# Kernel tuning notes

Measured on AMD Instinct MI355X. Metric: run time of the kernel, lower is better.

Reference implementation:

```python
import jax, jax.numpy as jnp
import numpy as np

W_OUT = 0.1     # weight for voxels outside the ROI
EXPAND = 1.2    # ROI expansion coefficient


def _compute_roi(mask):
    """Vectorized equivalent of MaskedLoss._compute_roi_ for 5D [B,1,D,H,W] masks.
    Returns roi of same shape: 1.0 inside the (expanded, clipped) bounding box of
    the foreground, W_OUT elsewhere (and everywhere if a batch item has no fg)."""
    m = mask[:, 0] > 0                      # [B, D, H, W] bool
    spatial = m.shape[1:]
    has_fg = jnp.any(m, axis=(1, 2, 3))     # [B]
    inside = []
    for ax, sh in enumerate(spatial):
        other = tuple(i + 1 for i in range(3) if i != ax)
        any_ax = jnp.any(m, axis=other)                     # [B, sh]
        mn = jnp.argmax(any_ax, axis=1).astype(jnp.float32)                      # first fg index
        mx = (sh - 1 - jnp.argmax(any_ax[:, ::-1], axis=1)).astype(jnp.float32)  # last fg index
        c = (mx + mn) * 0.5
        e = (mx - mn + 1.0) * 0.5 * EXPAND
        # int(max(0, c-e)) and int(min(sh-1, c+e)) with python int() truncation on >=0 values
        lo = jnp.maximum(0.0, jnp.floor(c - e))             # [B]
        hi = jnp.minimum(float(sh - 1), jnp.floor(c + e))   # [B], slice end is EXCLUSIVE
        coords = jnp.arange(sh, dtype=jnp.float32)
        inside.append((coords[None, :] >= lo[:, None]) & (coords[None, :] < hi[:, None]))
    box = (inside[0][:, :, None, None]
           & inside[1][:, None, :, None]
           & inside[2][:, None, None, :])                   # [B, D, H, W]
    box = box & has_fg[:, None, None, None]                 # no fg -> all W_OUT
    return jnp.where(box, 1.0, W_OUT)[:, None]              # [B, 1, D, H, W]


def setup_inputs() -> dict:
    key = jax.random.key(0)
    k1, k2, k3 = jax.random.split(key, 3)
    shape = (4, 1, 160, 160, 160)
    y_pred = jax.random.normal(k1, shape, dtype=jnp.float32)
    y_true = jax.random.normal(k2, shape, dtype=jnp.float32)
    mask = jax.random.randint(k3, shape, 0, 2, dtype=jnp.int32)
    return {"y_pred": y_pred, "y_true": y_true, "mask": mask}


def reference(y_pred, y_true, mask):
    roi = _compute_roi(mask)
    # func = MSE: mean((roi*pred - roi*true)^2)
    diff = roi * y_pred - roi * y_true
    return jnp.mean(diff * diff)
```

## Files before the change

kernel.cpp:

```cpp
#include <hip/hip_runtime.h>


namespace {
constexpr int BATCH = 4;
constexpr int DSZ = 160, HSZ = 160, WSZ = 160;
constexpr int SPATIAL = DSZ * HSZ * WSZ;
constexpr int QPB = SPATIAL / 4;
constexpr int NT = 256;
constexpr int PB = 500;
constexpr int STRIDE_Q = PB * NT;
constexpr int ITERS = QPB / STRIDE_Q;
constexpr int NPART = BATCH * PB;
constexpr int SENT_MIN = 1 << 30;
}

__device__ __forceinline__ int wred_min(int v) {
#pragma unroll
  for (int o = 32; o; o >>= 1) v = min(v, __shfl_xor(v, o));
  return v;
}
__device__ __forceinline__ int wred_max(int v) {
#pragma unroll
  for (int o = 32; o; o >>= 1) v = max(v, __shfl_xor(v, o));
  return v;
}

__global__ __launch_bounds__(NT) void ml_pass1(const int* __restrict__ mask,
                                               int* __restrict__ blockres) {
  const int b = blockIdx.y;
  const int4* m4 = reinterpret_cast<const int4*>(mask + (size_t)b * SPATIAL);

  const unsigned q0 = blockIdx.x * NT + threadIdx.x;
  const unsigned d0 = q0 / 6400u;
  const unsigned rem = q0 - d0 * 6400u;
  const unsigned h = rem / 40u;
  const int wb = (int)(rem - h * 40u) * 4;

  unsigned itermask = 0;
  int elemmask = 0;
#pragma unroll
  for (int i = 0; i < ITERS; ++i) {
    int4 v = m4[q0 + (size_t)i * STRIDE_Q];
    int e = (int)(v.x > 0) | ((int)(v.y > 0) << 1) |
            ((int)(v.z > 0) << 2) | ((int)(v.w > 0) << 3);
    elemmask |= e;
    itermask |= (e ? (1u << i) : 0u);
  }

  int dmin = SENT_MIN, dmax = -1, hmin = SENT_MIN, hmax = -1, wmin = SENT_MIN, wmax = -1;
  if (itermask) {
    int ifirst = __ffs(itermask) - 1;
    int ilast = 31 - __clz(itermask);
    dmin = (int)d0 + 20 * ifirst;
    dmax = (int)d0 + 20 * ilast;
    hmin = hmax = (int)h;
    wmin = wb + (__ffs(elemmask) - 1);
    wmax = wb + (31 - __clz(elemmask));
  }

  dmin = wred_min(dmin); dmax = wred_max(dmax);
  hmin = wred_min(hmin); hmax = wred_max(hmax);
  wmin = wred_min(wmin); wmax = wred_max(wmax);

  __shared__ int sred[4][6];
  const int wave = threadIdx.x >> 6, lane = threadIdx.x & 63;
  if (lane == 0) {
    sred[wave][0] = dmin; sred[wave][1] = dmax;
    sred[wave][2] = hmin; sred[wave][3] = hmax;
    sred[wave][4] = wmin; sred[wave][5] = wmax;
  }
  __syncthreads();
  if (threadIdx.x == 0) {
    int o[6];
    o[0] = min(min(sred[0][0], sred[1][0]), min(sred[2][0], sred[3][0]));
    o[1] = max(max(sred[0][1], sred[1][1]), max(sred[2][1], sred[3][1]));
    o[2] = min(min(sred[0][2], sred[1][2]), min(sred[2][2], sred[3][2]));
    o[3] = max(max(sred[0][3], sred[1][3]), max(sred[2][3], sred[3][3]));
    o[4] = min(min(sred[0][4], sred[1][4]), min(sred[2][4], sred[3][4]));
    o[5] = max(max(sred[0][5], sred[1][5]), max(sred[2][5], sred[3][5]));
    int* dst = blockres + ((size_t)b * PB + blockIdx.x) * 6;
#pragma unroll
    for (int k = 0; k < 6; ++k) dst[k] = o[k];
  }
}

__device__ __forceinline__ void axis_box(int mni, int mxi, int sh, int* lo_i, int* hi_i) {
  float mn = (float)mni, mx = (float)mxi;
  float c = (mx + mn) * 0.5f;
  float e = (mx - mn + 1.0f) * 0.5f * 1.2f;
  float lo = fmaxf(0.0f, floorf(c - e));
  float hi = fminf((float)(sh - 1), floorf(c + e));
  *lo_i = (int)lo;
  *hi_i = (int)hi;
}

__global__ __launch_bounds__(NT) void ml_pass2(const int* __restrict__ blockres,
                                               int* __restrict__ boxp) {
  const int b = blockIdx.x;
  int dmin = SENT_MIN, dmax = -1, hmin = SENT_MIN, hmax = -1, wmin = SENT_MIN, wmax = -1;
  for (int i = threadIdx.x; i < PB; i += NT) {
    const int* r = blockres + ((size_t)b * PB + i) * 6;
    dmin = min(dmin, r[0]); dmax = max(dmax, r[1]);
    hmin = min(hmin, r[2]); hmax = max(hmax, r[3]);
    wmin = min(wmin, r[4]); wmax = max(wmax, r[5]);
  }

  dmin = wred_min(dmin); dmax = wred_max(dmax);
  hmin = wred_min(hmin); hmax = wred_max(hmax);
  wmin = wred_min(wmin); wmax = wred_max(wmax);

  __shared__ int sred[4][6];
  const int wave = threadIdx.x >> 6, lane = threadIdx.x & 63;
  if (lane == 0) {
    sred[wave][0] = dmin; sred[wave][1] = dmax;
    sred[wave][2] = hmin; sred[wave][3] = hmax;
    sred[wave][4] = wmin; sred[wave][5] = wmax;
  }
  __syncthreads();
  if (threadIdx.x == 0) {
    int Dm = min(min(sred[0][0], sred[1][0]), min(sred[2][0], sred[3][0]));
    int DM = max(max(sred[0][1], sred[1][1]), max(sred[2][1], sred[3][1]));
    int Hm = min(min(sred[0][2], sred[1][2]), min(sred[2][2], sred[3][2]));
    int HM = max(max(sred[0][3], sred[1][3]), max(sred[2][3], sred[3][3]));
    int Wm = min(min(sred[0][4], sred[1][4]), min(sred[2][4], sred[3][4]));
    int WM = max(max(sred[0][5], sred[1][5]), max(sred[2][5], sred[3][5]));
    int out[6];
    if (DM < 0) {
      out[0] = 0; out[1] = 0; out[2] = 0; out[3] = 0; out[4] = 0; out[5] = 0;
    } else {
      axis_box(Dm, DM, DSZ, &out[0], &out[1]);
      axis_box(Hm, HM, HSZ, &out[2], &out[3]);
      axis_box(Wm, WM, WSZ, &out[4], &out[5]);
    }
    int* dst = boxp + b * 8;
#pragma unroll
    for (int k = 0; k < 6; ++k) dst[k] = out[k];
  }
}

__global__ __launch_bounds__(NT) void ml_pass3(const float* __restrict__ pred,
                                               const float* __restrict__ tru,
                                               const int* __restrict__ boxp,
                                               float* __restrict__ partials) {
  const int b = blockIdx.y;
  const int lod = boxp[b * 8 + 0], hid = boxp[b * 8 + 1];
  const int loh = boxp[b * 8 + 2], hih = boxp[b * 8 + 3];
  const int low = boxp[b * 8 + 4], hiw = boxp[b * 8 + 5];

  const float4* p4 = reinterpret_cast<const float4*>(pred + (size_t)b * SPATIAL);
  const float4* t4 = reinterpret_cast<const float4*>(tru + (size_t)b * SPATIAL);

  const unsigned q0 = blockIdx.x * NT + threadIdx.x;
  const unsigned d0 = q0 / 6400u;
  const unsigned rem = q0 - d0 * 6400u;
  const unsigned h = rem / 40u;
  const int wb = (int)(rem - h * 40u) * 4;

  const bool inh = ((int)h >= loh) & ((int)h < hih);
  const float wx = (inh & (wb + 0 >= low) & (wb + 0 < hiw)) ? 1.0f : 0.1f;
  const float wy = (inh & (wb + 1 >= low) & (wb + 1 < hiw)) ? 1.0f : 0.1f;
  const float wz = (inh & (wb + 2 >= low) & (wb + 2 < hiw)) ? 1.0f : 0.1f;
  const float ww = (inh & (wb + 3 >= low) & (wb + 3 < hiw)) ? 1.0f : 0.1f;

  float s0 = 0.0f, s1 = 0.0f, s2 = 0.0f, s3 = 0.0f;
#pragma unroll
  for (int i = 0; i < ITERS; ++i) {
    float4 pv = p4[q0 + (size_t)i * STRIDE_Q];
    float4 tv = t4[q0 + (size_t)i * STRIDE_Q];
    int d = (int)d0 + 20 * i;
    bool ind = (d >= lod) & (d < hid);
    float rx = ind ? wx : 0.1f;
    float ry = ind ? wy : 0.1f;
    float rz = ind ? wz : 0.1f;
    float rw = ind ? ww : 0.1f;
    float a;
    a = rx * pv.x - rx * tv.x; s0 = fmaf(a, a, s0);
    a = ry * pv.y - ry * tv.y; s1 = fmaf(a, a, s1);
    a = rz * pv.z - rz * tv.z; s2 = fmaf(a, a, s2);
    a = rw * pv.w - rw * tv.w; s3 = fmaf(a, a, s3);
  }
  float s = (s0 + s1) + (s2 + s3);

#pragma unroll
  for (int o = 32; o; o >>= 1) s += __shfl_xor(s, o);
  __shared__ float ls[4];
  const int wave = threadIdx.x >> 6, lane = threadIdx.x & 63;
  if (lane == 0) ls[wave] = s;
  __syncthreads();
  if (threadIdx.x == 0)
    partials[(size_t)b * PB + blockIdx.x] = ls[0] + ls[1] + ls[2] + ls[3];
}

__global__ __launch_bounds__(NT) void ml_final(const float* __restrict__ partials,
                                               float* __restrict__ out) {
  double s = 0.0;
  for (int i = threadIdx.x; i < NPART; i += NT) s += (double)partials[i];
#pragma unroll
  for (int o = 32; o; o >>= 1) s += __shfl_xor(s, o);
  __shared__ double ls[4];
  const int wave = threadIdx.x >> 6, lane = threadIdx.x & 63;
  if (lane == 0) ls[wave] = s;
  __syncthreads();
  if (threadIdx.x == 0)
    out[0] = (float)((ls[0] + ls[1] + ls[2] + ls[3]) / (double)((size_t)BATCH * SPATIAL));
}

extern "C" void kernel_launch(void* const* d_in, const int* in_sizes, int n_in,
                              void* d_out, int out_size, void* d_ws, size_t ws_size,
                              hipStream_t stream) {
  const float* y_pred = (const float*)d_in[0];
  const float* y_true = (const float*)d_in[1];
  const int*   mask   = (const int*)d_in[2];
  float* out = (float*)d_out;

  char* ws = (char*)d_ws;
  int*   blockres = (int*)(ws);
  int*   boxp     = (int*)(ws + 49152);
  float* partials = (float*)(ws + 53248);

  ml_pass1<<<dim3(PB, BATCH), NT, 0, stream>>>(mask, blockres);
  ml_pass2<<<dim3(BATCH), NT, 0, stream>>>(blockres, boxp);
  ml_pass3<<<dim3(PB, BATCH), NT, 0, stream>>>(y_pred, y_true, boxp, partials);
  ml_final<<<1, NT, 0, stream>>>(partials, out);
}
```

Measured before the change: 194.1 us.

## Fuse bbox reduction via atomics and final sum via last-block pattern

```diff
diff --git a/kernel.cpp b/kernel.cpp
--- a/kernel.cpp
+++ b/kernel.cpp
@@ -7,11 +7,28 @@
 constexpr int SPATIAL = DSZ * HSZ * WSZ;
 constexpr int QPB = SPATIAL / 4;
 constexpr int NT = 256;
-constexpr int PB = 500;
-constexpr int STRIDE_Q = PB * NT;
+constexpr int PB = 1000;
+constexpr int STRIDE_Q = PB * NT * 2;
 constexpr int ITERS = QPB / STRIDE_Q;
+constexpr int DSTEP = 80;
 constexpr int NPART = BATCH * PB;
+constexpr int TOTAL_BLOCKS = BATCH * PB;
 constexpr int SENT_MIN = 1 << 30;
+
+constexpr int WS_NEG = 0;
+constexpr int WS_MAX = 64;
+constexpr int WS_CNT = 128;
+constexpr int WS_PART = 256;
+}
+
+typedef int   vint4   __attribute__((ext_vector_type(4)));
+typedef float vfloat4 __attribute__((ext_vector_type(4)));
+
+__device__ __forceinline__ vint4 ntload_i(const vint4* p) {
+  return __builtin_nontemporal_load(p);
+}
+__device__ __forceinline__ vfloat4 ntload_f(const vfloat4* p) {
+  return __builtin_nontemporal_load(p);
 }
 
 __device__ __forceinline__ int wred_min(int v) {
@@ -25,14 +42,25 @@
   return v;
 }
 
-__global__ __launch_bounds__(NT) void ml_pass1(const int* __restrict__ mask,
-                                               int* __restrict__ blockres) {
+__global__ void ml_init(int* __restrict__ ws_i) {
+  if (threadIdx.x == 0) {
+#pragma unroll
+    for (int k = 0; k < 12; ++k) ws_i[k] = -1;
+#pragma unroll
+    for (int k = 0; k < 12; ++k) ws_i[16 + k] = -1;
+    ws_i[32] = 0;
+  }
+}
+
+__global__ __launch_bounds__(NT) void ml_bbox(const int* __restrict__ mask,
+                                              int* __restrict__ bneg,
+                                              int* __restrict__ bmax) {
   const int b = blockIdx.y;
-  const int4* m4 = reinterpret_cast<const int4*>(mask + (size_t)b * SPATIAL);
-
-  const unsigned q0 = blockIdx.x * NT + threadIdx.x;
-  const unsigned d0 = q0 / 6400u;
-  const unsigned rem = q0 - d0 * 6400u;
+  const vint4* m4 = reinterpret_cast<const vint4*>(mask + (size_t)b * SPATIAL);
+
+  const unsigned qb = (blockIdx.x * NT + threadIdx.x) * 2u;
+  const unsigned d0 = qb / 6400u;
+  const unsigned rem = qb - d0 * 6400u;
   const unsigned h = rem / 40u;
   const int wb = (int)(rem - h * 40u) * 4;
 
@@ -40,9 +68,12 @@
   int elemmask = 0;
 #pragma unroll
   for (int i = 0; i < ITERS; ++i) {
-    int4 v = m4[q0 + (size_t)i * STRIDE_Q];
-    int e = (int)(v.x > 0) | ((int)(v.y > 0) << 1) |
-            ((int)(v.z > 0) << 2) | ((int)(v.w > 0) << 3);
+    vint4 v0 = ntload_i(&m4[qb + (size_t)i * STRIDE_Q]);
+    vint4 v1 = ntload_i(&m4[qb + (size_t)i * STRIDE_Q + 1]);
+    int e = (int)(v0[0] > 0) | ((int)(v0[1] > 0) << 1) |
+            ((int)(v0[2] > 0) << 2) | ((int)(v0[3] > 0) << 3) |
+            ((int)(v1[0] > 0) << 4) | ((int)(v1[1] > 0) << 5) |
+            ((int)(v1[2] > 0) << 6) | ((int)(v1[3] > 0) << 7);
     elemmask |= e;
     itermask |= (e ? (1u << i) : 0u);
   }
@@ -51,8 +82,8 @@
   if (itermask) {
     int ifirst = __ffs(itermask) - 1;
     int ilast = 31 - __clz(itermask);
-    dmin = (int)d0 + 20 * ifirst;
-    dmax = (int)d0 + 20 * ilast;
+    dmin = (int)d0 + DSTEP * ifirst;
+    dmax = (int)d0 + DSTEP * ilast;
     hmin = hmax = (int)h;
     wmin = wb + (__ffs(elemmask) - 1);
     wmax = wb + (31 - __clz(elemmask));
@@ -71,16 +102,20 @@
   }
   __syncthreads();
   if (threadIdx.x == 0) {
-    int o[6];
-    o[0] = min(min(sred[0][0], sred[1][0]), min(sred[2][0], sred[3][0]));
-    o[1] = max(max(sred[0][1], sred[1][1]), max(sred[2][1], sred[3][1]));
-    o[2] = min(min(sred[0][2], sred[1][2]), min(sred[2][2], sred[3][2]));
-    o[3] = max(max(sred[0][3], sred[1][3]), max(sred[2][3], sred[3][3]));
-    o[4] = min(min(sred[0][4], sred[1][4]), min(sred[2][4], sred[3][4]));
-    o[5] = max(max(sred[0][5], sred[1][5]), max(sred[2][5], sred[3][5]));
-    int* dst = blockres + ((size_t)b * PB + blockIdx.x) * 6;
-#pragma unroll
-    for (int k = 0; k < 6; ++k) dst[k] = o[k];
+    int Dm = min(min(sred[0][0], sred[1][0]), min(sred[2][0], sred[3][0]));
+    int DM = max(max(sred[0][1], sred[1][1]), max(sred[2][1], sred[3][1]));
+    int Hm = min(min(sred[0][2], sred[1][2]), min(sred[2][2], sred[3][2]));
+    int HM = max(max(sred[0][3], sred[1][3]), max(sred[2][3], sred[3][3]));
+    int Wm = min(min(sred[0][4], sred[1][4]), min(sred[2][4], sred[3][4]));
+    int WM = max(max(sred[0][5], sred[1][5]), max(sred[2][5], sred[3][5]));
+    if (DM >= 0) {
+      atomicMax(&bneg[b * 3 + 0], (DSZ - 1) - Dm);
+      atomicMax(&bneg[b * 3 + 1], (HSZ - 1) - Hm);
+      atomicMax(&bneg[b * 3 + 2], (WSZ - 1) - Wm);
+      atomicMax(&bmax[b * 3 + 0], DM);
+      atomicMax(&bmax[b * 3 + 1], HM);
+      atomicMax(&bmax[b * 3 + 2], WM);
+    }
   }
 }
 
@@ -94,115 +129,90 @@
   *hi_i = (int)hi;
 }
 
-__global__ __launch_bounds__(NT) void ml_pass2(const int* __restrict__ blockres,
-                                               int* __restrict__ boxp) {
-  const int b = blockIdx.x;
-  int dmin = SENT_MIN, dmax = -1, hmin = SENT_MIN, hmax = -1, wmin = SENT_MIN, wmax = -1;
-  for (int i = threadIdx.x; i < PB; i += NT) {
-    const int* r = blockres + ((size_t)b * PB + i) * 6;
-    dmin = min(dmin, r[0]); dmax = max(dmax, r[1]);
-    hmin = min(hmin, r[2]); hmax = max(hmax, r[3]);
-    wmin = min(wmin, r[4]); wmax = max(wmax, r[5]);
-  }
-
-  dmin = wred_min(dmin); dmax = wred_max(dmax);
-  hmin = wred_min(hmin); hmax = wred_max(hmax);
-  wmin = wred_min(wmin); wmax = wred_max(wmax);
-
-  __shared__ int sred[4][6];
-  const int wave = threadIdx.x >> 6, lane = threadIdx.x & 63;
-  if (lane == 0) {
-    sred[wave][0] = dmin; sred[wave][1] = dmax;
-    sred[wave][2] = hmin; sred[wave][3] = hmax;
-    sred[wave][4] = wmin; sred[wave][5] = wmax;
-  }
-  __syncthreads();
-  if (threadIdx.x == 0) {
-    int Dm = min(min(sred[0][0], sred[1][0]), min(sred[2][0], sred[3][0]));
-    int DM = max(max(sred[0][1], sred[1][1]), max(sred[2][1], sred[3][1]));
-    int Hm = min(min(sred[0][2], sred[1][2]), min(sred[2][2], sred[3][2]));
-    int HM = max(max(sred[0][3], sred[1][3]), max(sred[2][3], sred[3][3]));
-    int Wm = min(min(sred[0][4], sred[1][4]), min(sred[2][4], sred[3][4]));
-    int WM = max(max(sred[0][5], sred[1][5]), max(sred[2][5], sred[3][5]));
-    int out[6];
-    if (DM < 0) {
-      out[0] = 0; out[1] = 0; out[2] = 0; out[3] = 0; out[4] = 0; out[5] = 0;
-    } else {
-      axis_box(Dm, DM, DSZ, &out[0], &out[1]);
-      axis_box(Hm, HM, HSZ, &out[2], &out[3]);
-      axis_box(Wm, WM, WSZ, &out[4], &out[5]);
-    }
-    int* dst = boxp + b * 8;
-#pragma unroll
-    for (int k = 0; k < 6; ++k) dst[k] = out[k];
-  }
-}
-
-__global__ __launch_bounds__(NT) void ml_pass3(const float* __restrict__ pred,
-                                               const float* __restrict__ tru,
-                                               const int* __restrict__ boxp,
-                                               float* __restrict__ partials) {
+__global__ __launch_bounds__(NT) void ml_loss(const float* __restrict__ pred,
+                                              const float* __restrict__ tru,
+                                              const int* __restrict__ bneg,
+                                              const int* __restrict__ bmax,
+                                              int* __restrict__ counter,
+                                              float* __restrict__ partials,
+                                              float* __restrict__ out) {
   const int b = blockIdx.y;
-  const int lod = boxp[b * 8 + 0], hid = boxp[b * 8 + 1];
-  const int loh = boxp[b * 8 + 2], hih = boxp[b * 8 + 3];
-  const int low = boxp[b * 8 + 4], hiw = boxp[b * 8 + 5];
-
-  const float4* p4 = reinterpret_cast<const float4*>(pred + (size_t)b * SPATIAL);
-  const float4* t4 = reinterpret_cast<const float4*>(tru + (size_t)b * SPATIAL);
-
-  const unsigned q0 = blockIdx.x * NT + threadIdx.x;
-  const unsigned d0 = q0 / 6400u;
-  const unsigned rem = q0 - d0 * 6400u;
+
+  const int DM = bmax[b * 3 + 0], HM = bmax[b * 3 + 1], WM = bmax[b * 3 + 2];
+  const int Dm = (DSZ - 1) - bneg[b * 3 + 0];
+  const int Hm = (HSZ - 1) - bneg[b * 3 + 1];
+  const int Wm = (WSZ - 1) - bneg[b * 3 + 2];
+  int lod = 0, hid = 0, loh = 0, hih = 0, low = 0, hiw = 0;
+  if (DM >= 0) {
+    axis_box(Dm, DM, DSZ, &lod, &hid);
+    axis_box(Hm, HM, HSZ, &loh, &hih);
+    axis_box(Wm, WM, WSZ, &low, &hiw);
+  }
+
+  const vfloat4* p4 = reinterpret_cast<const vfloat4*>(pred + (size_t)b * SPATIAL);
+  const vfloat4* t4 = reinterpret_cast<const vfloat4*>(tru + (size_t)b * SPATIAL);
+
+  const unsigned qb = (blockIdx.x * NT + threadIdx.x) * 2u;
+  const unsigned d0 = qb / 6400u;
+  const unsigned rem = qb - d0 * 6400u;
   const unsigned h = rem / 40u;
   const int wb = (int)(rem - h * 40u) * 4;
 
   const bool inh = ((int)h >= loh) & ((int)h < hih);
-  const float wx = (inh & (wb + 0 >= low) & (wb + 0 < hiw)) ? 1.0f : 0.1f;
-  const float wy = (inh & (wb + 1 >= low) & (wb + 1 < hiw)) ? 1.0f : 0.1f;
-  const float wz = (inh & (wb + 2 >= low) & (wb + 2 < hiw)) ? 1.0f : 0.1f;
-  const float ww = (inh & (wb + 3 >= low) & (wb + 3 < hiw)) ? 1.0f : 0.1f;
+  float wgt[8];
+#pragma unroll
+  for (int j = 0; j < 8; ++j)
+    wgt[j] = (inh & (wb + j >= low) & (wb + j < hiw)) ? 1.0f : 0.1f;
 
   float s0 = 0.0f, s1 = 0.0f, s2 = 0.0f, s3 = 0.0f;
 #pragma unroll
   for (int i = 0; i < ITERS; ++i) {
-    float4 pv = p4[q0 + (size_t)i * STRIDE_Q];
-    float4 tv = t4[q0 + (size_t)i * STRIDE_Q];
-    int d = (int)d0 + 20 * i;
-    bool ind = (d >= lod) & (d < hid);
-    float rx = ind ? wx : 0.1f;
-    float ry = ind ? wy : 0.1f;
-    float rz = ind ? wz : 0.1f;
-    float rw = ind ? ww : 0.1f;
-    float a;
-    a = rx * pv.x - rx * tv.x; s0 = fmaf(a, a, s0);
-    a = ry * pv.y - ry * tv.y; s1 = fmaf(a, a, s1);
-    a = rz * pv.z - rz * tv.z; s2 = fmaf(a, a, s2);
-    a = rw * pv.w - rw * tv.w; s3 = fmaf(a, a, s3);
+    const size_t q = qb + (size_t)i * STRIDE_Q;
+    vfloat4 pv0 = ntload_f(&p4[q]);
+    vfloat4 pv1 = ntload_f(&p4[q + 1]);
+    vfloat4 tv0 = ntload_f(&t4[q]);
+    vfloat4 tv1 = ntload_f(&t4[q + 1]);
+    const int d = (int)d0 + DSTEP * i;
+    const bool ind = (d >= lod) & (d < hid);
+    float r, a;
+    r = ind ? wgt[0] : 0.1f; a = r * pv0[0] - r * tv0[0]; s0 = fmaf(a, a, s0);
+    r = ind ? wgt[1] : 0.1f; a = r * pv0[1] - r * tv0[1]; s1 = fmaf(a, a, s1);
+    r = ind ? wgt[2] : 0.1f; a = r * pv0[2] - r * tv0[2]; s2 = fmaf(a, a, s2);
+    r = ind ? wgt[3] : 0.1f; a = r * pv0[3] - r * tv0[3]; s3 = fmaf(a, a, s3);
+    r = ind ? wgt[4] : 0.1f; a = r * pv1[0] - r * tv1[0]; s0 = fmaf(a, a, s0);
+    r = ind ? wgt[5] : 0.1f; a = r * pv1[1] - r * tv1[1]; s1 = fmaf(a, a, s1);
+    r = ind ? wgt[6] : 0.1f; a = r * pv1[2] - r * tv1[2]; s2 = fmaf(a, a, s2);
+    r = ind ? wgt[7] : 0.1f; a = r * pv1[3] - r * tv1[3]; s3 = fmaf(a, a, s3);
   }
   float s = (s0 + s1) + (s2 + s3);
 
 #pragma unroll
   for (int o = 32; o; o >>= 1) s += __shfl_xor(s, o);
   __shared__ float ls[4];
+  __shared__ bool amLast;
   const int wave = threadIdx.x >> 6, lane = threadIdx.x & 63;
   if (lane == 0) ls[wave] = s;
   __syncthreads();
-  if (threadIdx.x == 0)
+  if (threadIdx.x == 0) {
     partials[(size_t)b * PB + blockIdx.x] = ls[0] + ls[1] + ls[2] + ls[3];
-}
-
-__global__ __launch_bounds__(NT) void ml_final(const float* __restrict__ partials,
-                                               float* __restrict__ out) {
-  double s = 0.0;
-  for (int i = threadIdx.x; i < NPART; i += NT) s += (double)partials[i];
-#pragma unroll
-  for (int o = 32; o; o >>= 1) s += __shfl_xor(s, o);
-  __shared__ double ls[4];
-  const int wave = threadIdx.x >> 6, lane = threadIdx.x & 63;
-  if (lane == 0) ls[wave] = s;
+    __threadfence();
+    int old = atomicAdd(counter, 1);
+    amLast = (old == TOTAL_BLOCKS - 1);
+  }
   __syncthreads();
-  if (threadIdx.x == 0)
-    out[0] = (float)((ls[0] + ls[1] + ls[2] + ls[3]) / (double)((size_t)BATCH * SPATIAL));
+
+  if (amLast) {
+    __threadfence();
+    double acc = 0.0;
+    for (int i = threadIdx.x; i < NPART; i += NT) acc += (double)partials[i];
+#pragma unroll
+    for (int o = 32; o; o >>= 1) acc += __shfl_xor(acc, o);
+    __shared__ double ld[4];
+    if (lane == 0) ld[wave] = acc;
+    __syncthreads();
+    if (threadIdx.x == 0)
+      out[0] = (float)((ld[0] + ld[1] + ld[2] + ld[3]) / (double)((size_t)BATCH * SPATIAL));
+  }
 }
 
 extern "C" void kernel_launch(void* const* d_in, const int* in_sizes, int n_in,
@@ -214,12 +224,13 @@
   float* out = (float*)d_out;
 
   char* ws = (char*)d_ws;
-  int*   blockres = (int*)(ws);
-  int*   boxp     = (int*)(ws + 49152);
-  float* partials = (float*)(ws + 53248);
-
-  ml_pass1<<<dim3(PB, BATCH), NT, 0, stream>>>(mask, blockres);
-  ml_pass2<<<dim3(BATCH), NT, 0, stream>>>(blockres, boxp);
-  ml_pass3<<<dim3(PB, BATCH), NT, 0, stream>>>(y_pred, y_true, boxp, partials);
-  ml_final<<<1, NT, 0, stream>>>(partials, out);
-}
+  int*   bneg     = (int*)(ws + WS_NEG);
+  int*   bmax     = (int*)(ws + WS_MAX);
+  int*   counter  = (int*)(ws + WS_CNT);
+  float* partials = (float*)(ws + WS_PART);
+
+  ml_init<<<1, 64, 0, stream>>>((int*)ws);
+  ml_bbox<<<dim3(PB, BATCH), NT, 0, stream>>>(mask, bneg, bmax);
+  ml_loss<<<dim3(PB, BATCH), NT, 0, stream>>>(y_pred, y_true, bneg, bmax,
+                                              counter, partials, out);
+}
```

Measured after the change: 521.8 us. 2.69x slower.
